# Kernel optimization log

Hardware: AMD Instinct MI355X
Metric: run time of the kernel (lower is better)

Reference implementation:

```python
import jax, jax.numpy as jnp
import numpy as np

B, L, D = 16, 4096, 512
WORD_SIZE = 2048  # codebook_size // 4
WORD_LEN = 2


def setup_inputs() -> dict:
    key = jax.random.key(0)
    k1, k2, k3, k4, k5 = jax.random.split(key, 5)
    char_tokens = jax.random.randint(k1, (B, L), 0, 8192, dtype=jnp.int64 if jax.config.jax_enable_x64 else jnp.int32)
    char_embeddings = jax.random.normal(k2, (B, L, D), dtype=jnp.float32)
    # word_codebook initialized uniform(-1/word_size, 1/word_size) in the original
    word_codebook = jax.random.uniform(k3, (WORD_SIZE, D), dtype=jnp.float32,
                                       minval=-1.0 / WORD_SIZE, maxval=1.0 / WORD_SIZE)
    proj_w = jax.random.normal(k4, (D, D), dtype=jnp.float32) * (1.0 / np.sqrt(D))
    proj_b = jax.random.normal(k5, (D,), dtype=jnp.float32) * 0.01
    return {"char_tokens": char_tokens, "char_embeddings": char_embeddings,
            "word_codebook": word_codebook, "proj_w": proj_w, "proj_b": proj_b}


def reference(char_tokens, char_embeddings, word_codebook, proj_w, proj_b):
    Bv, Lv, Dv = char_embeddings.shape
    G = Lv // WORD_LEN  # number of 2-char groups per sequence
    # mean-pool each consecutive pair of characters -> [B, G, D]
    means = char_embeddings.reshape(Bv, G, WORD_LEN, Dv).mean(axis=2)
    # squared-euclidean nearest codebook entry (same argmin as cdist)
    # d2[b,g,k] = ||m||^2 - 2 m.W^T + ||W||^2 ; ||m||^2 constant over k -> drop
    dots = jnp.einsum('bgd,kd->bgk', means, word_codebook)            # [B,G,K]
    cb_sq = jnp.sum(word_codebook * word_codebook, axis=-1)           # [K]
    word_indices = jnp.argmin(cb_sq[None, None, :] - 2.0 * dots, axis=-1)  # [B,G]
    word_embeddings = word_codebook[word_indices]                     # [B,G,D]
    # alignment loss: mse(proj(word_emb), stop_grad(word_emb))
    projected = jnp.einsum('bgd,ed->bge', word_embeddings, proj_w) + proj_b
    target = jax.lax.stop_gradient(word_embeddings)
    alignment_loss = jnp.mean((projected - target) ** 2)
    return (word_indices, word_embeddings, alignment_loss)
```

## Files before the change

### kernel.cpp

```cpp
#include <hip/hip_runtime.h>


#define D_DIM    512
#define K_CODES  2048
#define N_ROWS   32768
#define EPS_GAP  1e-5f
#define LOSS_SCALE (1.0f / 16777216.0f)

typedef __attribute__((ext_vector_type(8))) short short8;
typedef __attribute__((ext_vector_type(4))) float f32x4;

__device__ __forceinline__ void split_bf16(float f, unsigned short& h, unsigned short& l) {
    unsigned u = __float_as_uint(f);
    h = (unsigned short)(u >> 16);
    float hr = __uint_as_float(u & 0xFFFF0000u);
    l = (unsigned short)(__float_as_uint(f - hr) >> 16);
}

__device__ __forceinline__ void dma16(const void* g, void* l) {
    __builtin_amdgcn_global_load_lds(
        (const __attribute__((address_space(1))) unsigned int*)g,
        (__attribute__((address_space(3))) unsigned int*)l, 16, 0, 0);
}

__device__ __forceinline__ void merge_cand(float s, int idx, float& v1, int& i1, float& v2, int& i2) {
    if (s < v1 || (s == v1 && idx < i1)) { v2 = v1; i2 = i1; v1 = s; i1 = idx; }
    else if (s < v2 || (s == v2 && idx < i2)) { v2 = s; i2 = idx; }
}

__global__ __launch_bounds__(256, 1)
void cra_pack_a(const float* __restrict__ ce,
                unsigned short* __restrict__ Ap)
{
    const int tid = threadIdx.x;
    const int mb  = blockIdx.x;
    const int rq  = tid >> 5;
    const int dq  = tid & 31;
    const int dbase = dq * 16;
    const int ach = dq >> 1;
    const int k0  = (dq & 1) * 16;

    #pragma unroll 2
    for (int p = 0; p < 16; ++p) {
        const int r  = p * 8 + rq;
        const int gr = mb * 128 + r;
        const float* a0 = ce + (size_t)(2 * gr) * D_DIM + dbase;
        const float* a1 = a0 + D_DIM;
        float4 x0[4], x1[4];
        #pragma unroll
        for (int q = 0; q < 4; ++q) {
            x0[q] = *(const float4*)(a0 + q * 4);
            x1[q] = *(const float4*)(a1 + q * 4);
        }
        short8 h8[2], l8[2];
        #pragma unroll
        for (int q = 0; q < 4; ++q) {
            const float m[4] = {0.5f * (x0[q].x + x1[q].x), 0.5f * (x0[q].y + x1[q].y),
                                0.5f * (x0[q].z + x1[q].z), 0.5f * (x0[q].w + x1[q].w)};
            #pragma unroll
            for (int e = 0; e < 4; ++e) {
                unsigned short hh, ll;
                split_bf16(m[e], hh, ll);
                h8[q >> 1][(q & 1) * 4 + e] = (short)hh;
                l8[q >> 1][(q & 1) * 4 + e] = (short)ll;
            }
        }
        const size_t hb = ((size_t)(mb * 32 + ach) * 128 + r) * 32 + k0;
        const size_t lb = ((size_t)(mb * 32 + 16 + ach) * 128 + r) * 32 + k0;
        *(short8*)(Ap + hb)     = h8[0];
        *(short8*)(Ap + hb + 8) = h8[1];
        *(short8*)(Ap + lb)     = l8[0];
        *(short8*)(Ap + lb + 8) = l8[1];
    }
}

__global__ __launch_bounds__(256, 1)
void cra_pack_b(const float* __restrict__ cb,
                unsigned short* __restrict__ Bp,
                float* __restrict__ cb_sq,
                float* __restrict__ Sk,
                int* __restrict__ counter,
                float* __restrict__ loss_out)
{
    __shared__ float cbs[32 * D_DIM];
    const int tid = threadIdx.x;
    const int c0  = blockIdx.x * 32;

    if (blockIdx.x == 0) {
        #pragma unroll
        for (int j = 0; j < 8; ++j) Sk[tid + j * 256] = 0.0f;
        if (tid == 0) { counter[0] = 0; loss_out[0] = 0.0f; }
    }

    {
        const float4* src = (const float4*)(cb + (size_t)c0 * D_DIM);
        float4* dst = (float4*)cbs;
        #pragma unroll
        for (int k = 0; k < 16; ++k) dst[tid + k * 256] = src[tid + k * 256];
    }
    __syncthreads();

    if (tid < 32) {
        const float* r = cbs + tid * D_DIM;
        float s = 0.f;
        for (int d = 0; d < D_DIM; ++d) s = fmaf(r[d], r[d], s);
        cb_sq[c0 + tid] = s;
    }

    const int row  = tid >> 3;
    const int k    = c0 + row;
    const int colb = k >> 7;
    const int pr   = k & 127;
    const int dspan = (tid & 7) * 64;
    #pragma unroll
    for (int g = 0; g < 8; ++g) {
        const int d   = dspan + g * 8;
        const int bch = d >> 5;
        const int k0  = d & 31;
        short8 h8, l8;
        #pragma unroll
        for (int e = 0; e < 8; ++e) {
            unsigned short hh, ll;
            split_bf16(cbs[row * D_DIM + d + e], hh, ll);
            h8[e] = (short)hh; l8[e] = (short)ll;
        }
        *(short8*)(Bp + ((size_t)(colb * 32 + bch) * 128 + pr) * 32 + k0)      = h8;
        *(short8*)(Bp + ((size_t)(colb * 32 + 16 + bch) * 128 + pr) * 32 + k0) = l8;
    }
}

__global__ __launch_bounds__(256, 1)
void cra_proj(const float* __restrict__ cb,
              const float* __restrict__ W,
              const float* __restrict__ pb,
              float* __restrict__ Sk)
{
    __shared__ float cbs[32 * D_DIM];
    __shared__ float red[4 * 32];
    const int tid = threadIdx.x;
    const int cblock = blockIdx.x >> 2;
    const int eb     = blockIdx.x & 3;
    const int c0 = cblock * 32;

    {
        const float4* src = (const float4*)(cb + (size_t)c0 * D_DIM);
        float4* dst = (float4*)cbs;
        #pragma unroll
        for (int k = 0; k < 16; ++k) dst[tid + k * 256] = src[tid + k * 256];
    }
    __syncthreads();

    const int e  = eb * 128 + (tid >> 1);
    const int dh = (tid & 1) * 256;
    float acc[32];
    #pragma unroll
    for (int c = 0; c < 32; ++c) acc[c] = 0.f;
    const float4* wrow = (const float4*)(W + (size_t)e * D_DIM + dh);
    for (int dq = 0; dq < 64; ++dq) {
        const float4 wv = wrow[dq];
        #pragma unroll
        for (int c = 0; c < 32; ++c) {
            const float4 cv = *(const float4*)&cbs[c * D_DIM + dh + dq * 4];
            acc[c] += cv.x * wv.x + cv.y * wv.y + cv.z * wv.z + cv.w * wv.w;
        }
    }
    const float bias = pb[e];
    const int w = tid >> 6;
    #pragma unroll
    for (int c = 0; c < 32; ++c) {
        const float full = acc[c] + __shfl_xor(acc[c], 1);
        const float diff = full + bias - cbs[c * D_DIM + e];
        float v = (tid & 1) ? 0.f : diff * diff;
        #pragma unroll
        for (int off = 32; off > 0; off >>= 1) v += __shfl_down(v, off, 64);
        if ((tid & 63) == 0) red[w * 32 + c] = v;
    }
    __syncthreads();
    if (tid < 32)
        atomicAdd(&Sk[c0 + tid],
                  red[tid] + red[32 + tid] + red[64 + tid] + red[96 + tid]);
}

__global__ __launch_bounds__(256, 3)
void cra_gemm(const unsigned short* __restrict__ Ap,
              const unsigned short* __restrict__ Bp,
              const float* __restrict__ cb_sq,
              float4* __restrict__ wsRed)
{
    __shared__ short sMem[3 * 8192];

    const int tid  = threadIdx.x;
    const int bid  = blockIdx.x;
    const int xcd  = bid & 7;
    const int slot = bid >> 3;
    const int mb   = xcd * 32 + (slot >> 4);
    const int colb = slot & 15;
    const int rowBase = mb * 128;
    const int colBase = colb * 128;

    const int lane = tid & 63;
    const int w    = tid >> 6;
    const int wr   = (w & 1) * 64;
    const int wcH  = w >> 1;
    const int wc   = wcH * 64;
    const int cid  = lane & 15;
    const int quad = lane >> 4;

    f32x4 acc[4][4];
    #pragma unroll
    for (int i = 0; i < 4; ++i)
        #pragma unroll
        for (int j = 0; j < 4; ++j) acc[i][j] = (f32x4)(0.f);

    const char* Ag = (const char*)Ap + ((size_t)mb   * 32) * 8192 + w * 2048 + lane * 16;
    const char* Bg = (const char*)Bp + ((size_t)colb * 32) * 8192 + w * 2048 + lane * 16;

    auto stage = [&](int g, int p) {
        const int ach = g & 31;
        const int bch = (g & 15) | ((g & 32) >> 1);
        const char* ag = Ag + ach * 8192;
        const char* bg = Bg + bch * 8192;
        char* lA = (char*)sMem + p * 16384 + w * 2048;
        char* lB = lA + 8192;
        dma16(ag,        lA);
        dma16(ag + 1024, lA + 1024);
        dma16(bg,        lB);
        dma16(bg + 1024, lB + 1024);
    };

    stage(0, 0);
    stage(1, 1);

    int p  = 0;
    int pn = 2;
    #pragma unroll 1
    for (int g = 0; g < 48; ++g) {
        if (g < 47) asm volatile("s_waitcnt vmcnt(4)\n\ts_barrier" ::: "memory");
        else        asm volatile("s_waitcnt vmcnt(0)\n\ts_barrier" ::: "memory");

        const short* sA = sMem + p * 8192;
        const short* sB = sA + 4096;

        short8 aF[4], bF[4];
        #pragma unroll
        for (int mi = 0; mi < 4; ++mi) aF[mi] = *(const short8*)&sA[(wr + mi * 16 + cid) * 32 + quad * 8];
        #pragma unroll
        for (int ni = 0; ni < 4; ++ni) bF[ni] = *(const short8*)&sB[(wc + ni * 16 + cid) * 32 + quad * 8];
        __builtin_amdgcn_s_setprio(1);
        #pragma unroll
        for (int mi = 0; mi < 4; ++mi)
            #pragma unroll
            for (int ni = 0; ni < 4; ++ni)
                acc[mi][ni] = __builtin_amdgcn_mfma_f32_16x16x32_bf16(aF[mi], bF[ni], acc[mi][ni], 0, 0, 0);
        __builtin_amdgcn_s_setprio(0);

        asm volatile("s_waitcnt lgkmcnt(0)\n\ts_barrier" ::: "memory");

        if (g + 2 < 48) stage(g + 2, pn);
        p  = (p  == 2) ? 0 : p  + 1;
        pn = (pn == 2) ? 0 : pn + 1;
    }

    float cq[4];
    #pragma unroll
    for (int ni = 0; ni < 4; ++ni) cq[ni] = cb_sq[colBase + wc + ni * 16 + cid];

    float4* sRed = (float4*)sMem;
    #pragma unroll
    for (int mi = 0; mi < 4; ++mi) {
        #pragma unroll
        for (int reg = 0; reg < 4; ++reg) {
            float v1 = 3.4e38f, v2 = 3.4e38f;
            int   i1 = 0x7FFFFFFF, i2 = 0x7FFFFFFF;
            #pragma unroll
            for (int ni = 0; ni < 4; ++ni) {
                const float s = fmaf(-2.0f, acc[mi][ni][reg], cq[ni]);
                merge_cand(s, colBase + wc + ni * 16 + cid, v1, i1, v2, i2);
            }
            #pragma unroll
            for (int d = 1; d <= 2; d <<= 1) {
                float ov1 = __shfl_xor(v1, d); int oi1 = __shfl_xor(i1, d);
                float ov2 = __shfl_xor(v2, d); int oi2 = __shfl_xor(i2, d);
                merge_cand(ov1, oi1, v1, i1, v2, i2);
                merge_cand(ov2, oi2, v1, i1, v2, i2);
            }
            if ((cid & 3) == 0) {
                const int row = wr + mi * 16 + quad * 4 + reg;
                sRed[(row * 2 + wcH) * 4 + (cid >> 2)] =
                    make_float4(v1, __int_as_float(i1), v2, __int_as_float(i2));
            }
        }
    }
    __syncthreads();
    if (tid < 128) {
        float v1 = 3.4e38f, v2 = 3.4e38f;
        int   i1 = 0x7FFFFFFF, i2 = 0x7FFFFFFF;
        #pragma unroll
        for (int e = 0; e < 8; ++e) {
            const float4 t = sRed[tid * 8 + e];
            merge_cand(t.x, __float_as_int(t.y), v1, i1, v2, i2);
            merge_cand(t.z, __float_as_int(t.w), v1, i1, v2, i2);
        }
        wsRed[(size_t)(rowBase + tid) * 16 + colb] =
            make_float4(v1, __int_as_float(i1), v2, __int_as_float(i2));
    }
}

__global__ __launch_bounds__(256, 1)
void cra_merge(const float4* __restrict__ wsRed,
               const float* __restrict__ Sk,
               float* __restrict__ out_idx,
               float* __restrict__ out_loss,
               int* __restrict__ counter,
               int* __restrict__ flagRow,
               int2* __restrict__ flagI)
{
    __shared__ float sl[256];
    const int tid = threadIdx.x;
    const int r = blockIdx.x * 256 + tid;
    float v1 = 3.4e38f, v2 = 3.4e38f;
    int   i1 = 0x7FFFFFFF, i2 = 0x7FFFFFFF;
    #pragma unroll 4
    for (int cbk = 0; cbk < 16; ++cbk) {
        const float4 t = wsRed[(size_t)r * 16 + cbk];
        merge_cand(t.x, __float_as_int(t.y), v1, i1, v2, i2);
        merge_cand(t.z, __float_as_int(t.w), v1, i1, v2, i2);
    }
    out_idx[r] = (float)i1;
    if (v2 - v1 < EPS_GAP) {
        const int slot = atomicAdd(counter, 1);
        flagRow[slot] = r;
        flagI[slot] = make_int2(i1, i2);
    }
    sl[tid] = Sk[i1];
    __syncthreads();
    for (int s = 128; s > 0; s >>= 1) { if (tid < s) sl[tid] += sl[tid + s]; __syncthreads(); }
    if (tid == 0) atomicAdd(out_loss, sl[0] * LOSS_SCALE);
}

__global__ __launch_bounds__(256, 1)
void cra_gather(const float* __restrict__ out_idx,
                const float4* __restrict__ cb4,
                float4* __restrict__ out4)
{
    __shared__ int sidx[128];
    const int tid = threadIdx.x;
    const int rb = blockIdx.x * 128;
    if (tid < 128) sidx[tid] = (int)out_idx[rb + tid];
    __syncthreads();
    for (int j = tid; j < 128 * 128; j += 256) {
        const int row = j >> 7, q = j & 127;
        out4[(size_t)(rb + row) * 128 + q] = cb4[(size_t)sidx[row] * 128 + q];
    }
}

__global__ __launch_bounds__(256, 1)
void cra_recheck(const float* __restrict__ ce,
                 const float* __restrict__ cb,
                 const float* __restrict__ cb_sq,
                 const float* __restrict__ Sk,
                 const int* __restrict__ counter,
                 const int* __restrict__ flagRow,
                 const int2* __restrict__ flagI,
                 float* __restrict__ out_idx,
                 float4* __restrict__ out4,
                 float* __restrict__ out_loss,
                 const float4* __restrict__ cb4)
{
    __shared__ float rp[8];
    __shared__ int swin;
    const int tid = threadIdx.x;
    const int n = counter[0];
    for (int f = blockIdx.x; f < n; f += 64) {
        const int row = flagRow[f];
        const int2 ii = flagI[f];
        const int d0 = tid * 2;
        const float2 x0 = *(const float2*)(ce + (size_t)(2 * row) * D_DIM + d0);
        const float2 x1 = *(const float2*)(ce + (size_t)(2 * row) * D_DIM + D_DIM + d0);
        const float m0 = 0.5f * (x0.x + x1.x), m1 = 0.5f * (x0.y + x1.y);
        const float* c1 = cb + (size_t)ii.x * D_DIM + d0;
        const float* c2 = cb + (size_t)ii.y * D_DIM + d0;
        float p1 = fmaf(m0, c1[0], m1 * c1[1]);
        float p2 = fmaf(m0, c2[0], m1 * c2[1]);
        #pragma unroll
        for (int off = 32; off > 0; off >>= 1) {
            p1 += __shfl_down(p1, off, 64);
            p2 += __shfl_down(p2, off, 64);
        }
        if ((tid & 63) == 0) { rp[(tid >> 6) * 2] = p1; rp[(tid >> 6) * 2 + 1] = p2; }
        __syncthreads();
        if (tid == 0) {
            const float dot1 = rp[0] + rp[2] + rp[4] + rp[6];
            const float dot2 = rp[1] + rp[3] + rp[5] + rp[7];
            const float s1 = cb_sq[ii.x] - 2.f * dot1;
            const float s2 = cb_sq[ii.y] - 2.f * dot2;
            const int win = (s2 < s1 || (s2 == s1 && ii.y < ii.x)) ? ii.y : ii.x;
            swin = win;
            if (win != ii.x) {
                out_idx[row] = (float)win;
                atomicAdd(out_loss, (Sk[win] - Sk[ii.x]) * LOSS_SCALE);
            }
        }
        __syncthreads();
        if (swin != ii.x) {
            for (int q = tid; q < 128; q += 256)
                out4[(size_t)row * 128 + q] = cb4[(size_t)swin * 128 + q];
        }
        __syncthreads();
    }
}

extern "C" void kernel_launch(void* const* d_in, const int* in_sizes, int n_in,
                              void* d_out, int out_size, void* d_ws, size_t ws_size,
                              hipStream_t stream)
{
    const float* ce = (const float*)d_in[1];
    const float* cb = (const float*)d_in[2];
    const float* W  = (const float*)d_in[3];
    const float* pb = (const float*)d_in[4];

    char* ws = (char*)d_ws;
    unsigned short* Bp = (unsigned short*)ws;
    float4* wsRed  = (float4*)(ws + 4194304);
    float* cb_sq   = (float*)(ws + 12582912);
    float* Sk      = (float*)(ws + 12582912 + 8192);
    int*   flagRow = (int*)(ws + 12582912 + 16384);
    int2*  flagI   = (int2*)(ws + 12582912 + 16384 + 131072);
    int*   counter = (int*)(ws + 12582912 + 16384 + 131072 + 262144);

    float* out_idx  = (float*)d_out;
    float* out_emb  = out_idx + N_ROWS;
    float* out_loss = out_emb + (size_t)N_ROWS * D_DIM;
    unsigned short* Ap = (unsigned short*)out_emb;

    cra_pack_a<<<256, 256, 0, stream>>>(ce, Ap);
    cra_pack_b<<<64, 256, 0, stream>>>(cb, Bp, cb_sq, Sk, counter, out_loss);
    cra_proj<<<256, 256, 0, stream>>>(cb, W, pb, Sk);
    cra_gemm<<<4096, 256, 0, stream>>>(Ap, Bp, cb_sq, wsRed);
    cra_merge<<<128, 256, 0, stream>>>(wsRed, Sk, out_idx, out_loss, counter, flagRow, flagI);
    cra_gather<<<256, 256, 0, stream>>>(out_idx, (const float4*)cb, (float4*)out_emb);
    cra_recheck<<<64, 256, 0, stream>>>(ce, cb, cb_sq, Sk, counter, flagRow, flagI,
                                        out_idx, (float4*)out_emb, out_loss, (const float4*)cb);
}
```

Before: 932.4 us.

## Enlarge GEMM tile to 256x256 with 1024-thread workgroups and double buffering

```diff
diff --git a/kernel.cpp b/kernel.cpp
--- a/kernel.cpp
+++ b/kernel.cpp
@@ -181,71 +181,72 @@
                   red[tid] + red[32 + tid] + red[64 + tid] + red[96 + tid]);
 }
 
-__global__ __launch_bounds__(256, 3)
+__global__ __launch_bounds__(1024, 4)
 void cra_gemm(const unsigned short* __restrict__ Ap,
               const unsigned short* __restrict__ Bp,
               const float* __restrict__ cb_sq,
               float4* __restrict__ wsRed)
 {
-    __shared__ short sMem[3 * 8192];
+    __shared__ __align__(16) char sMem[65536];
 
     const int tid  = threadIdx.x;
     const int bid  = blockIdx.x;
-    const int xcd  = bid & 7;
-    const int slot = bid >> 3;
-    const int mb   = xcd * 32 + (slot >> 4);
-    const int colb = slot & 15;
-    const int rowBase = mb * 128;
-    const int colBase = colb * 128;
+    const int wgid = (bid & 7) * 128 + (bid >> 3);
+    const int mb   = wgid >> 3;
+    const int colb = wgid & 7;
+    const int rowBase = mb * 256;
+    const int colBase = colb * 256;
 
     const int lane = tid & 63;
     const int w    = tid >> 6;
-    const int wr   = (w & 1) * 64;
-    const int wcH  = w >> 1;
-    const int wc   = wcH * 64;
+    const int wm   = w >> 2;
+    const int wn   = w & 3;
     const int cid  = lane & 15;
     const int quad = lane >> 4;
 
+    const int rg  = w >> 2;
+    const int off = (w & 3) * 2048;
+    const char* AgBase = (const char*)Ap + ((size_t)(2 * mb)   * 32) * 8192 + lane * 16;
+    const char* BgBase = (const char*)Bp + ((size_t)(2 * colb) * 32) * 8192 + lane * 16;
+    const char* gBase  = (rg < 2) ? (AgBase + (rg & 1) * (32 * 8192) + off)
+                                  : (BgBase + (rg & 1) * (32 * 8192) + off);
+    const int dstOff = (rg >> 1) * 16384 + (rg & 1) * 8192 + off;
+
     f32x4 acc[4][4];
     #pragma unroll
     for (int i = 0; i < 4; ++i)
         #pragma unroll
         for (int j = 0; j < 4; ++j) acc[i][j] = (f32x4)(0.f);
-
-    const char* Ag = (const char*)Ap + ((size_t)mb   * 32) * 8192 + w * 2048 + lane * 16;
-    const char* Bg = (const char*)Bp + ((size_t)colb * 32) * 8192 + w * 2048 + lane * 16;
 
     auto stage = [&](int g, int p) {
         const int ach = g & 31;
         const int bch = (g & 15) | ((g & 32) >> 1);
-        const char* ag = Ag + ach * 8192;
-        const char* bg = Bg + bch * 8192;
-        char* lA = (char*)sMem + p * 16384 + w * 2048;
-        char* lB = lA + 8192;
-        dma16(ag,        lA);
-        dma16(ag + 1024, lA + 1024);
-        dma16(bg,        lB);
-        dma16(bg + 1024, lB + 1024);
+        const int ch  = (rg < 2) ? ach : bch;
+        const char* src = gBase + ch * 8192;
+        char* dst = (char*)sMem + p * 32768 + dstOff;
+        dma16(src,        dst);
+        dma16(src + 1024, dst + 1024);
     };
 
     stage(0, 0);
     stage(1, 1);
 
-    int p  = 0;
-    int pn = 2;
     #pragma unroll 1
     for (int g = 0; g < 48; ++g) {
-        if (g < 47) asm volatile("s_waitcnt vmcnt(4)\n\ts_barrier" ::: "memory");
+        const int p = g & 1;
+        if (g < 47) asm volatile("s_waitcnt vmcnt(2)\n\ts_barrier" ::: "memory");
         else        asm volatile("s_waitcnt vmcnt(0)\n\ts_barrier" ::: "memory");
 
-        const short* sA = sMem + p * 8192;
-        const short* sB = sA + 4096;
+        const short* sA = (const short*)(sMem + p * 32768);
+        const short* sB = (const short*)(sMem + p * 32768 + 16384);
 
         short8 aF[4], bF[4];
         #pragma unroll
-        for (int mi = 0; mi < 4; ++mi) aF[mi] = *(const short8*)&sA[(wr + mi * 16 + cid) * 32 + quad * 8];
-        #pragma unroll
-        for (int ni = 0; ni < 4; ++ni) bF[ni] = *(const short8*)&sB[(wc + ni * 16 + cid) * 32 + quad * 8];
+        for (int mi = 0; mi < 4; ++mi)
+            aF[mi] = *(const short8*)&sA[(wm * 64 + mi * 16 + cid) * 32 + quad * 8];
+        #pragma unroll
+        for (int ni = 0; ni < 4; ++ni)
+            bF[ni] = *(const short8*)&sB[(wn * 64 + ni * 16 + cid) * 32 + quad * 8];
         __builtin_amdgcn_s_setprio(1);
         #pragma unroll
         for (int mi = 0; mi < 4; ++mi)
@@ -256,14 +257,12 @@
 
         asm volatile("s_waitcnt lgkmcnt(0)\n\ts_barrier" ::: "memory");
 
-        if (g + 2 < 48) stage(g + 2, pn);
-        p  = (p  == 2) ? 0 : p  + 1;
-        pn = (pn == 2) ? 0 : pn + 1;
+        if (g + 2 < 48) stage(g + 2, p);
     }
 
     float cq[4];
     #pragma unroll
-    for (int ni = 0; ni < 4; ++ni) cq[ni] = cb_sq[colBase + wc + ni * 16 + cid];
+    for (int ni = 0; ni < 4; ++ni) cq[ni] = cb_sq[colBase + wn * 64 + ni * 16 + cid];
 
     float4* sRed = (float4*)sMem;
     #pragma unroll
@@ -275,7 +274,7 @@
             #pragma unroll
             for (int ni = 0; ni < 4; ++ni) {
                 const float s = fmaf(-2.0f, acc[mi][ni][reg], cq[ni]);
-                merge_cand(s, colBase + wc + ni * 16 + cid, v1, i1, v2, i2);
+                merge_cand(s, colBase + wn * 64 + ni * 16 + cid, v1, i1, v2, i2);
             }
             #pragma unroll
             for (int d = 1; d <= 2; d <<= 1) {
@@ -285,23 +284,23 @@
                 merge_cand(ov2, oi2, v1, i1, v2, i2);
             }
             if ((cid & 3) == 0) {
-                const int row = wr + mi * 16 + quad * 4 + reg;
-                sRed[(row * 2 + wcH) * 4 + (cid >> 2)] =
+                const int rl = wm * 64 + mi * 16 + quad * 4 + reg;
+                sRed[(rl * 4 + wn) * 4 + (cid >> 2)] =
                     make_float4(v1, __int_as_float(i1), v2, __int_as_float(i2));
             }
         }
     }
     __syncthreads();
-    if (tid < 128) {
+    if (tid < 256) {
         float v1 = 3.4e38f, v2 = 3.4e38f;
         int   i1 = 0x7FFFFFFF, i2 = 0x7FFFFFFF;
         #pragma unroll
-        for (int e = 0; e < 8; ++e) {
-            const float4 t = sRed[tid * 8 + e];
+        for (int e = 0; e < 16; ++e) {
+            const float4 t = sRed[tid * 16 + e];
             merge_cand(t.x, __float_as_int(t.y), v1, i1, v2, i2);
             merge_cand(t.z, __float_as_int(t.w), v1, i1, v2, i2);
         }
-        wsRed[(size_t)(rowBase + tid) * 16 + colb] =
+        wsRed[(size_t)(rowBase + tid) * 8 + colb] =
             make_float4(v1, __int_as_float(i1), v2, __int_as_float(i2));
     }
 }
@@ -321,8 +320,8 @@
     float v1 = 3.4e38f, v2 = 3.4e38f;
     int   i1 = 0x7FFFFFFF, i2 = 0x7FFFFFFF;
     #pragma unroll 4
-    for (int cbk = 0; cbk < 16; ++cbk) {
-        const float4 t = wsRed[(size_t)r * 16 + cbk];
+    for (int cbk = 0; cbk < 8; ++cbk) {
+        const float4 t = wsRed[(size_t)r * 8 + cbk];
         merge_cand(t.x, __float_as_int(t.y), v1, i1, v2, i2);
         merge_cand(t.z, __float_as_int(t.w), v1, i1, v2, i2);
     }
@@ -436,7 +435,7 @@
     cra_pack_a<<<256, 256, 0, stream>>>(ce, Ap);
     cra_pack_b<<<64, 256, 0, stream>>>(cb, Bp, cb_sq, Sk, counter, out_loss);
     cra_proj<<<256, 256, 0, stream>>>(cb, W, pb, Sk);
-    cra_gemm<<<4096, 256, 0, stream>>>(Ap, Bp, cb_sq, wsRed);
+    cra_gemm<<<1024, 1024, 0, stream>>>(Ap, Bp, cb_sq, wsRed);
     cra_merge<<<128, 256, 0, stream>>>(wsRed, Sk, out_idx, out_loss, counter, flagRow, flagI);
     cra_gather<<<256, 256, 0, stream>>>(out_idx, (const float4*)cb, (float4*)out_emb);
     cra_recheck<<<64, 256, 0, stream>>>(ce, cb, cb_sq, Sk, counter, flagRow, flagI,
```

Result: no change. 938.6 us (+0.7%).
